# Kernel tuning notes

Measured on AMD Instinct MI355X. Metric: run time of the kernel, lower is better.

The kernel has to match this reference:

```python
import jax, jax.numpy as jnp
import numpy as np

B, C, H, DK = 4, 5, 200, 20   # batch, cdd_length, his_length, projected dim
D_INNER = 400                 # Linear(400,1) fan-in


def setup_inputs() -> dict:
    key = jax.random.key(0)
    ks = jax.random.split(key, 8)
    Q = jax.random.normal(ks[0], (B, C, H, D_INNER, DK), jnp.float32)
    K = jax.random.normal(ks[1], (B, C, H, D_INNER, DK), jnp.float32)
    V = jax.random.normal(ks[2], (B, C, H, D_INNER, DK), jnp.float32)
    cdd = jax.random.normal(ks[3], (B, C, H, DK, DK), jnp.float32)
    # nn.Linear(400,1) weight/bias (weight stored as a vector of fan-in size)
    W = jax.random.normal(ks[4], (D_INNER,), jnp.float32) / np.sqrt(D_INNER)
    b = jax.random.normal(ks[5], (), jnp.float32) * 0.01
    # nn.Linear(20,1)
    W1 = jax.random.normal(ks[6], (DK,), jnp.float32) / np.sqrt(DK)
    b1 = jax.random.normal(ks[7], (), jnp.float32) * 0.01
    return {"Q": Q, "K": K, "V": V, "cdd": cdd, "W": W, "b": b, "W1": W1, "b1": b1, "d_k": DK}


def reference(Q, K, V, cdd, W, b, W1, b1, d_k):
    Bs, Cs, Hs = Q.shape[:3]

    def proj(x, w, bb):
        # x.view(B,C,H,-1,20).transpose(-1,-2) -> [B,C,H,20,n]; Linear(n,1).squeeze(-1) -> [B,C,H,20]
        x = x.reshape(Bs, Cs, Hs, -1, 20)       # [B,C,H,n,20]
        x = jnp.swapaxes(x, -1, -2)             # [B,C,H,20,n]
        return jnp.einsum('bchdn,n->bchd', x, w) + bb

    q = proj(Q, W, b)      # [B,C,H,20]
    k = proj(K, W, b)
    v = proj(V, W, b)
    c = proj(cdd, W1, b1)  # [B,C,H,20]

    inv_sqrt_dk = 1.0 / jnp.sqrt(jnp.float32(d_k))
    # scores1 = Q K^T, scores2 = K cdd^T over the his_length axis -> [B,C,H,H]
    scores = (jnp.einsum('bchd,bcgd->bchg', q, k)
              + jnp.einsum('bchd,bcgd->bchg', k, c)) * inv_sqrt_dk
    s = jnp.exp(scores)                                    # no max-subtraction, as in source
    attn = s / (jnp.sum(s, axis=-1, keepdims=True) + 1e-8)
    context = jnp.einsum('bchg,bcgd->bchd', attn, v)       # [B,C,H,20]
    return context, attn
```

## Files before the change

### kernel.cpp

```cpp
#include <hip/hip_runtime.h>

#define BB 4
#define CC 5
#define HH 200
#define DKk 20
#define DI 400
#define NPOS (BB*CC*HH)

__global__ __launch_bounds__(256) void proj_kernel(
    const float* __restrict__ Q,
    const float* __restrict__ K,
    const float* __restrict__ V,
    const float* __restrict__ cdd,
    const float* __restrict__ W,
    const float* __restrict__ bptr,
    const float* __restrict__ W1,
    const float* __restrict__ b1ptr,
    float* __restrict__ proj)
{
    __shared__ float sW[DI];
    __shared__ float sW1[DKk];
    for (int i = threadIdx.x; i < DI; i += 256) sW[i] = W[i];
    if (threadIdx.x < DKk) sW1[threadIdx.x] = W1[threadIdx.x];
    __syncthreads();

    const int tensor = threadIdx.x >> 6;
    const int lane   = threadIdx.x & 63;
    const int pos    = blockIdx.x;

    int rj[5], qj[5];
    #pragma unroll
    for (int j = 0; j < 5; ++j) {
        rj[j] = (64 * j + lane) / 5;
        qj[j] = (lane + 4 * j) % 5;
    }

    float4 acc[5];
    #pragma unroll
    for (int q = 0; q < 5; ++q) acc[q] = float4{0.f, 0.f, 0.f, 0.f};

#define ACCUM(xv, wnv, qv)                                                   \
    {                                                                        \
        float w0_ = (qv == 0) ? (wnv) : 0.f;                                 \
        float w1_ = (qv == 1) ? (wnv) : 0.f;                                 \
        float w2_ = (qv == 2) ? (wnv) : 0.f;                                 \
        float w3_ = (qv == 3) ? (wnv) : 0.f;                                 \
        float w4_ = (qv == 4) ? (wnv) : 0.f;                                 \
        acc[0].x += w0_ * xv.x; acc[0].y += w0_ * xv.y;                      \
        acc[0].z += w0_ * xv.z; acc[0].w += w0_ * xv.w;                      \
        acc[1].x += w1_ * xv.x; acc[1].y += w1_ * xv.y;                      \
        acc[1].z += w1_ * xv.z; acc[1].w += w1_ * xv.w;                      \
        acc[2].x += w2_ * xv.x; acc[2].y += w2_ * xv.y;                      \
        acc[2].z += w2_ * xv.z; acc[2].w += w2_ * xv.w;                      \
        acc[3].x += w3_ * xv.x; acc[3].y += w3_ * xv.y;                      \
        acc[3].z += w3_ * xv.z; acc[3].w += w3_ * xv.w;                      \
        acc[4].x += w4_ * xv.x; acc[4].y += w4_ * xv.y;                      \
        acc[4].z += w4_ * xv.z; acc[4].w += w4_ * xv.w;                      \
    }

    if (tensor < 3) {
        const float4* src = reinterpret_cast<const float4*>(
            ((tensor == 0) ? Q : (tensor == 1) ? K : V) + (size_t)pos * (DI * DKk));

        for (int g = 0; g < 6; ++g) {
            float4 x[5];
            #pragma unroll
            for (int j = 0; j < 5; ++j)
                x[j] = src[320 * g + 64 * j + lane];
            float wns[5];
            #pragma unroll
            for (int j = 0; j < 5; ++j)
                wns[j] = sW[64 * g + rj[j]];
            #pragma unroll
            for (int j = 0; j < 5; ++j)
                ACCUM(x[j], wns[j], qj[j]);
        }
        {
            float4 x0 = src[320 * 6 + lane];
            float wn0 = sW[384 + rj[0]];
            ACCUM(x0, wn0, qj[0]);
            if (lane < 16) {
                float4 x1 = src[320 * 6 + 64 + lane];
                float wn1 = sW[384 + rj[1]];
                ACCUM(x1, wn1, qj[1]);
            }
        }
    } else {
        const float4* src = reinterpret_cast<const float4*>(
            cdd + (size_t)pos * (DKk * DKk));
        float4 x0 = src[lane];
        float wn0 = sW1[rj[0]];
        ACCUM(x0, wn0, qj[0]);
        if (lane < 36) {
            float4 x1 = src[64 + lane];
            float wn1 = sW1[rj[1]];
            ACCUM(x1, wn1, qj[1]);
        }
    }
#undef ACCUM

    #pragma unroll
    for (int m = 32; m >= 1; m >>= 1) {
        #pragma unroll
        for (int q = 0; q < 5; ++q) {
            acc[q].x += __shfl_xor(acc[q].x, m);
            acc[q].y += __shfl_xor(acc[q].y, m);
            acc[q].z += __shfl_xor(acc[q].z, m);
            acc[q].w += __shfl_xor(acc[q].w, m);
        }
    }

    if (lane == 0) {
        const float bias = (tensor < 3) ? bptr[0] : b1ptr[0];
        float4* dst = reinterpret_cast<float4*>(
            proj + ((size_t)tensor * NPOS + pos) * DKk);
        #pragma unroll
        for (int q = 0; q < 5; ++q) {
            float4 o;
            o.x = acc[q].x + bias;
            o.y = acc[q].y + bias;
            o.z = acc[q].z + bias;
            o.w = acc[q].w + bias;
            dst[q] = o;
        }
    }
}

__global__ __launch_bounds__(256) void attn_kernel(
    const float* __restrict__ proj,
    float* __restrict__ attn_out,
    float* __restrict__ ctx_out)
{
    __shared__ float sk[HH * DKk];
    __shared__ float sc[HH * DKk];
    __shared__ float sv[HH * DKk];

    int bc   = blockIdx.x / 50;
    int tile = blockIdx.x % 50;
    int t    = threadIdx.x;

    const float* kp = proj + ((size_t)1 * NPOS + bc * HH) * DKk;
    const float* vp = proj + ((size_t)2 * NPOS + bc * HH) * DKk;
    const float* cp = proj + ((size_t)3 * NPOS + bc * HH) * DKk;

    for (int i = t; i < HH * DKk / 4; i += 256) {
        reinterpret_cast<float4*>(sk)[i] = reinterpret_cast<const float4*>(kp)[i];
        reinterpret_cast<float4*>(sc)[i] = reinterpret_cast<const float4*>(cp)[i];
        reinterpret_cast<float4*>(sv)[i] = reinterpret_cast<const float4*>(vp)[i];
    }
    __syncthreads();

    int row = t >> 6;
    int sub = t & 63;
    int h   = tile * 4 + row;
    int rowIdx = bc * HH + h;

    const float* qr_p = proj + ((size_t)0 * NPOS + rowIdx) * DKk;
    const float* kr_p = proj + ((size_t)1 * NPOS + rowIdx) * DKk;
    float qr[DKk], kr[DKk];
    #pragma unroll
    for (int i = 0; i < 5; ++i) {
        float4 a = reinterpret_cast<const float4*>(qr_p)[i];
        qr[4*i] = a.x; qr[4*i+1] = a.y; qr[4*i+2] = a.z; qr[4*i+3] = a.w;
        float4 b = reinterpret_cast<const float4*>(kr_p)[i];
        kr[4*i] = b.x; kr[4*i+1] = b.y; kr[4*i+2] = b.z; kr[4*i+3] = b.w;
    }

    const float inv_sqrt = 0.22360679774997896f;
    float ctx[DKk];
    #pragma unroll
    for (int d = 0; d < DKk; ++d) ctx[d] = 0.f;
    float rs = 0.f;
    float sreg[4];

    #pragma unroll
    for (int kk = 0; kk < 4; ++kk) {
        int g = sub + 64 * kk;
        float s = 0.f;
        if (g < HH) {
            float dot = 0.f;
            #pragma unroll
            for (int i = 0; i < 5; ++i) {
                float4 kg = reinterpret_cast<const float4*>(sk + g * DKk)[i];
                float4 cg = reinterpret_cast<const float4*>(sc + g * DKk)[i];
                dot += qr[4*i]   * kg.x + qr[4*i+1] * kg.y
                     + qr[4*i+2] * kg.z + qr[4*i+3] * kg.w;
                dot += kr[4*i]   * cg.x + kr[4*i+1] * cg.y
                     + kr[4*i+2] * cg.z + kr[4*i+3] * cg.w;
            }
            s = __expf(dot * inv_sqrt);
            #pragma unroll
            for (int i = 0; i < 5; ++i) {
                float4 vg = reinterpret_cast<const float4*>(sv + g * DKk)[i];
                ctx[4*i]   += s * vg.x;
                ctx[4*i+1] += s * vg.y;
                ctx[4*i+2] += s * vg.z;
                ctx[4*i+3] += s * vg.w;
            }
        }
        sreg[kk] = s;
        rs += s;
    }

    #pragma unroll
    for (int off = 32; off >= 1; off >>= 1)
        rs += __shfl_xor(rs, off);
    float inv = 1.0f / (rs + 1e-8f);

    #pragma unroll
    for (int off = 32; off >= 1; off >>= 1) {
        #pragma unroll
        for (int d = 0; d < DKk; ++d)
            ctx[d] += __shfl_xor(ctx[d], off);
    }

    if (sub == 0) {
        float* co = ctx_out + (size_t)rowIdx * DKk;
        #pragma unroll
        for (int i = 0; i < 5; ++i) {
            float4 o;
            o.x = ctx[4*i]   * inv;
            o.y = ctx[4*i+1] * inv;
            o.z = ctx[4*i+2] * inv;
            o.w = ctx[4*i+3] * inv;
            reinterpret_cast<float4*>(co)[i] = o;
        }
    }

    #pragma unroll
    for (int kk = 0; kk < 4; ++kk) {
        int g = sub + 64 * kk;
        if (g < HH)
            attn_out[(size_t)rowIdx * HH + g] = sreg[kk] * inv;
    }
}

extern "C" void kernel_launch(void* const* d_in, const int* in_sizes, int n_in,
                              void* d_out, int out_size, void* d_ws, size_t ws_size,
                              hipStream_t stream) {
    const float* Q   = (const float*)d_in[0];
    const float* K   = (const float*)d_in[1];
    const float* V   = (const float*)d_in[2];
    const float* cdd = (const float*)d_in[3];
    const float* W   = (const float*)d_in[4];
    const float* b   = (const float*)d_in[5];
    const float* W1  = (const float*)d_in[6];
    const float* b1  = (const float*)d_in[7];

    float* proj = (float*)d_ws;

    float* out      = (float*)d_out;
    float* ctx_out  = out;
    float* attn_out = out + 80000;

    proj_kernel<<<NPOS, 256, 0, stream>>>(
        Q, K, V, cdd, W, b, W1, b1, proj);
    attn_kernel<<<CC * BB * 50, 256, 0, stream>>>(proj, attn_out, ctx_out);
}
```

Before: 376.0 us.

## Split projection into per-tensor blocks with direct global-to-LDS loads

After: 373.5 us. Within noise of the previous version (-0.7%).

```diff
diff --git a/kernel.cpp b/kernel.cpp
--- a/kernel.cpp
+++ b/kernel.cpp
@@ -6,98 +6,90 @@
 #define DKk 20
 #define DI 400
 #define NPOS (BB*CC*HH)
-
-__global__ __launch_bounds__(256) void proj_kernel(
+#define TILE_F4 2000
+#define TILE_PAD 2048
+
+__device__ __forceinline__ void load_to_lds16(const void* g, void* l) {
+    __builtin_amdgcn_global_load_lds(
+        (const __attribute__((address_space(1))) unsigned int*)g,
+        (__attribute__((address_space(3))) unsigned int*)l, 16, 0, 0);
+}
+
+#define ACCUM(xv, wnv, qv)                                                   \
+    {                                                                        \
+        float w0_ = ((qv) == 0) ? (wnv) : 0.f;                               \
+        float w1_ = ((qv) == 1) ? (wnv) : 0.f;                               \
+        float w2_ = ((qv) == 2) ? (wnv) : 0.f;                               \
+        float w3_ = ((qv) == 3) ? (wnv) : 0.f;                               \
+        float w4_ = ((qv) == 4) ? (wnv) : 0.f;                               \
+        acc[0].x += w0_ * (xv).x; acc[0].y += w0_ * (xv).y;                  \
+        acc[0].z += w0_ * (xv).z; acc[0].w += w0_ * (xv).w;                  \
+        acc[1].x += w1_ * (xv).x; acc[1].y += w1_ * (xv).y;                  \
+        acc[1].z += w1_ * (xv).z; acc[1].w += w1_ * (xv).w;                  \
+        acc[2].x += w2_ * (xv).x; acc[2].y += w2_ * (xv).y;                  \
+        acc[2].z += w2_ * (xv).z; acc[2].w += w2_ * (xv).w;                  \
+        acc[3].x += w3_ * (xv).x; acc[3].y += w3_ * (xv).y;                  \
+        acc[3].z += w3_ * (xv).z; acc[3].w += w3_ * (xv).w;                  \
+        acc[4].x += w4_ * (xv).x; acc[4].y += w4_ * (xv).y;                  \
+        acc[4].z += w4_ * (xv).z; acc[4].w += w4_ * (xv).w;                  \
+    }
+
+__global__ __launch_bounds__(256) void proj_qkv_kernel(
     const float* __restrict__ Q,
     const float* __restrict__ K,
     const float* __restrict__ V,
-    const float* __restrict__ cdd,
     const float* __restrict__ W,
     const float* __restrict__ bptr,
-    const float* __restrict__ W1,
-    const float* __restrict__ b1ptr,
     float* __restrict__ proj)
 {
-    __shared__ float sW[DI];
-    __shared__ float sW1[DKk];
-    for (int i = threadIdx.x; i < DI; i += 256) sW[i] = W[i];
-    if (threadIdx.x < DKk) sW1[threadIdx.x] = W1[threadIdx.x];
+    __shared__ float4 tile[TILE_PAD];
+    __shared__ float  sW[DI];
+    __shared__ float  red[4][DKk];
+
+    const int t    = threadIdx.x;
+    const int wave = t >> 6;
+    const int lane = t & 63;
+    const int tensor = blockIdx.x / NPOS;
+    const int pos    = blockIdx.x % NPOS;
+
+    const float* base = (tensor == 0) ? Q : (tensor == 1) ? K : V;
+    const float4* gsrc = reinterpret_cast<const float4*>(
+        base + (size_t)pos * (DI * DKk));
+
+    for (int i = t; i < DI; i += 256) sW[i] = W[i];
+
+    #pragma unroll
+    for (int r = 0; r < 8; ++r) {
+        int idx = r * 256 + t;
+        int cidx = (idx < TILE_F4) ? idx : (TILE_F4 - 1);
+        load_to_lds16((const void*)(gsrc + cidx),
+                      (void*)(tile + r * 256 + wave * 64));
+    }
     __syncthreads();
 
-    const int tensor = threadIdx.x >> 6;
-    const int lane   = threadIdx.x & 63;
-    const int pos    = blockIdx.x;
-
-    int rj[5], qj[5];
-    #pragma unroll
-    for (int j = 0; j < 5; ++j) {
-        rj[j] = (64 * j + lane) / 5;
-        qj[j] = (lane + 4 * j) % 5;
-    }
-
     float4 acc[5];
     #pragma unroll
     for (int q = 0; q < 5; ++q) acc[q] = float4{0.f, 0.f, 0.f, 0.f};
-
-#define ACCUM(xv, wnv, qv)                                                   \
-    {                                                                        \
-        float w0_ = (qv == 0) ? (wnv) : 0.f;                                 \
-        float w1_ = (qv == 1) ? (wnv) : 0.f;                                 \
-        float w2_ = (qv == 2) ? (wnv) : 0.f;                                 \
-        float w3_ = (qv == 3) ? (wnv) : 0.f;                                 \
-        float w4_ = (qv == 4) ? (wnv) : 0.f;                                 \
-        acc[0].x += w0_ * xv.x; acc[0].y += w0_ * xv.y;                      \
-        acc[0].z += w0_ * xv.z; acc[0].w += w0_ * xv.w;                      \
-        acc[1].x += w1_ * xv.x; acc[1].y += w1_ * xv.y;                      \
-        acc[1].z += w1_ * xv.z; acc[1].w += w1_ * xv.w;                      \
-        acc[2].x += w2_ * xv.x; acc[2].y += w2_ * xv.y;                      \
-        acc[2].z += w2_ * xv.z; acc[2].w += w2_ * xv.w;                      \
-        acc[3].x += w3_ * xv.x; acc[3].y += w3_ * xv.y;                      \
-        acc[3].z += w3_ * xv.z; acc[3].w += w3_ * xv.w;                      \
-        acc[4].x += w4_ * xv.x; acc[4].y += w4_ * xv.y;                      \
-        acc[4].z += w4_ * xv.z; acc[4].w += w4_ * xv.w;                      \
-    }
-
-    if (tensor < 3) {
-        const float4* src = reinterpret_cast<const float4*>(
-            ((tensor == 0) ? Q : (tensor == 1) ? K : V) + (size_t)pos * (DI * DKk));
-
-        for (int g = 0; g < 6; ++g) {
-            float4 x[5];
-            #pragma unroll
-            for (int j = 0; j < 5; ++j)
-                x[j] = src[320 * g + 64 * j + lane];
-            float wns[5];
-            #pragma unroll
-            for (int j = 0; j < 5; ++j)
-                wns[j] = sW[64 * g + rj[j]];
-            #pragma unroll
-            for (int j = 0; j < 5; ++j)
-                ACCUM(x[j], wns[j], qj[j]);
-        }
-        {
-            float4 x0 = src[320 * 6 + lane];
-            float wn0 = sW[384 + rj[0]];
-            ACCUM(x0, wn0, qj[0]);
-            if (lane < 16) {
-                float4 x1 = src[320 * 6 + 64 + lane];
-                float wn1 = sW[384 + rj[1]];
-                ACCUM(x1, wn1, qj[1]);
-            }
-        }
-    } else {
-        const float4* src = reinterpret_cast<const float4*>(
-            cdd + (size_t)pos * (DKk * DKk));
-        float4 x0 = src[lane];
-        float wn0 = sW1[rj[0]];
-        ACCUM(x0, wn0, qj[0]);
-        if (lane < 36) {
-            float4 x1 = src[64 + lane];
-            float wn1 = sW1[rj[1]];
-            ACCUM(x1, wn1, qj[1]);
-        }
-    }
-#undef ACCUM
+    const int q0 = t % 5;
+
+    float4 xs[7];
+    float  wns[7];
+    #pragma unroll
+    for (int r = 0; r < 7; ++r) xs[r] = tile[r * 256 + t];
+    #pragma unroll
+    for (int r = 0; r < 7; ++r) wns[r] = sW[(r * 256 + t) / 5];
+    #pragma unroll
+    for (int r = 0; r < 7; ++r) {
+        int q = q0 + r; if (q >= 5) q -= 5; if (q >= 5) q -= 5;
+        ACCUM(xs[r], wns[r], q);
+    }
+    if (t < TILE_F4 - 7 * 256) {
+        int idx = 7 * 256 + t;
+        float4 x = tile[idx];
+        float wn = sW[idx / 5];
+        int q = q0 + 7; if (q >= 5) q -= 5; if (q >= 5) q -= 5;
+        ACCUM(x, wn, q);
+    }
 
     #pragma unroll
     for (int m = 32; m >= 1; m >>= 1) {
@@ -109,11 +101,66 @@
             acc[q].w += __shfl_xor(acc[q].w, m);
         }
     }
-
     if (lane == 0) {
-        const float bias = (tensor < 3) ? bptr[0] : b1ptr[0];
+        #pragma unroll
+        for (int q = 0; q < 5; ++q) {
+            red[wave][4*q+0] = acc[q].x;
+            red[wave][4*q+1] = acc[q].y;
+            red[wave][4*q+2] = acc[q].z;
+            red[wave][4*q+3] = acc[q].w;
+        }
+    }
+    __syncthreads();
+    if (t < DKk) {
+        float s = red[0][t] + red[1][t] + red[2][t] + red[3][t] + bptr[0];
+        proj[((size_t)tensor * NPOS + pos) * DKk + t] = s;
+    }
+}
+
+__global__ __launch_bounds__(256) void proj_cdd_kernel(
+    const float* __restrict__ cdd,
+    const float* __restrict__ W1,
+    const float* __restrict__ b1ptr,
+    float* __restrict__ proj)
+{
+    const int wave = threadIdx.x >> 6;
+    const int lane = threadIdx.x & 63;
+    const int pos  = blockIdx.x * 4 + wave;
+
+    int rj0 = lane / 5,        qj0 = lane % 5;
+    int rj1 = (64 + lane) / 5, qj1 = (lane + 4) % 5;
+
+    float4 acc[5];
+    #pragma unroll
+    for (int q = 0; q < 5; ++q) acc[q] = float4{0.f, 0.f, 0.f, 0.f};
+
+    const float4* src = reinterpret_cast<const float4*>(
+        cdd + (size_t)pos * (DKk * DKk));
+    {
+        float4 x0 = src[lane];
+        float wn0 = W1[rj0];
+        ACCUM(x0, wn0, qj0);
+    }
+    if (lane < 36) {
+        float4 x1 = src[64 + lane];
+        float wn1 = W1[rj1];
+        ACCUM(x1, wn1, qj1);
+    }
+
+    #pragma unroll
+    for (int m = 32; m >= 1; m >>= 1) {
+        #pragma unroll
+        for (int q = 0; q < 5; ++q) {
+            acc[q].x += __shfl_xor(acc[q].x, m);
+            acc[q].y += __shfl_xor(acc[q].y, m);
+            acc[q].z += __shfl_xor(acc[q].z, m);
+            acc[q].w += __shfl_xor(acc[q].w, m);
+        }
+    }
+    if (lane == 0) {
+        const float bias = b1ptr[0];
         float4* dst = reinterpret_cast<float4*>(
-            proj + ((size_t)tensor * NPOS + pos) * DKk);
+            proj + ((size_t)3 * NPOS + pos) * DKk);
         #pragma unroll
         for (int q = 0; q < 5; ++q) {
             float4 o;
@@ -253,7 +300,7 @@
     float* ctx_out  = out;
     float* attn_out = out + 80000;
 
-    proj_kernel<<<NPOS, 256, 0, stream>>>(
-        Q, K, V, cdd, W, b, W1, b1, proj);
+    proj_qkv_kernel<<<3 * NPOS, 256, 0, stream>>>(Q, K, V, W, b, proj);
+    proj_cdd_kernel<<<NPOS / 4, 256, 0, stream>>>(cdd, W1, b1, proj);
     attn_kernel<<<CC * BB * 50, 256, 0, stream>>>(proj, attn_out, ctx_out);
 }
```
